# Kernel optimization log

Hardware: AMD Instinct MI355X
Metric: run time of the kernel (lower is better)

The kernel has to match this reference:

```python
import jax, jax.numpy as jnp
import numpy as np

B, H, N, D, M = 1, 4, 2048, 64, 256  # batch, heads, seq, dim_heads, nb_features
EPS = 1e-4


def _gaussian_orthogonal_random_matrix(nb_rows, nb_cols, seed=0):
    # scaling=1 path of the torch code: stacked transposed-Q orthogonal blocks,
    # scaled by sqrt(nb_cols).
    rng = np.random.default_rng(seed)
    blocks = []
    for _ in range(nb_rows // nb_cols):
        q, _ = np.linalg.qr(rng.standard_normal((nb_cols, nb_cols)))
        blocks.append(q.T)
    final = np.concatenate(blocks, axis=0)  # [nb_rows, nb_cols]
    return jnp.asarray(np.sqrt(float(nb_cols)) * final, dtype=jnp.float32)


def setup_inputs() -> dict:
    key = jax.random.key(0)
    kq, kk, kv = jax.random.split(key, 3)
    return {
        "q": jax.random.normal(kq, (B, H, N, D), dtype=jnp.float32),
        "k": jax.random.normal(kk, (B, H, N, D), dtype=jnp.float32),
        "v": jax.random.normal(kv, (B, H, N, D), dtype=jnp.float32),
        "projection_matrix": _gaussian_orthogonal_random_matrix(M, D),
    }


def _softmax_kernel(data, projection_matrix, is_query):
    # data: [B,H,N,D], projection_matrix: [M,D] -> features [B,H,N,M]
    data_normalizer = 1.0 / data.shape[-1] ** 0.25
    ratio = 1.0 / projection_matrix.shape[0] ** 0.5
    data_dash = jnp.einsum("bhnd,md->bhnm", data_normalizer * data, projection_matrix)
    diag_data = jnp.sum(data * data, axis=-1) * 0.5 * data_normalizer ** 2  # [B,H,N]
    diag_data = diag_data[..., None]  # [B,H,N,1]
    if is_query:
        stab = jnp.max(data_dash, axis=-1, keepdims=True)
    else:
        stab = jnp.max(data_dash)
    return ratio * (jnp.exp(data_dash - diag_data - stab) + EPS)


def _causal_linear_attention(q, k, v):
    # q,k: [B,H,N,M] features; v: [B,H,N,E]
    k_cumsum = jnp.cumsum(k, axis=-2)                       # [B,H,N,M]
    context = jnp.einsum("bhnm,bhne->bhnme", k, v)          # outer products
    context = jnp.cumsum(context, axis=-3)                  # cumulative over n
    context = context / k_cumsum[..., None]                 # [B,H,N,M,E]
    return jnp.einsum("bhnme,bhnm->bhne", context, q)


def reference(q, k, v, projection_matrix):
    q_feat = _softmax_kernel(q, projection_matrix, is_query=True)
    k_feat = _softmax_kernel(k, projection_matrix, is_query=False)
    return _causal_linear_attention(q_feat, k_feat, v)
```

## Files before the change

### kernel.cpp

```cpp
#include <hip/hip_runtime.h>
#include <math.h>

#define NH   4
#define SEQ  2048
#define DH   64
#define NF   256
#define ROWS (NH*SEQ)
#define DN    0.35355339059327373f
#define DIAGC 0.0625f
#define RATIO 0.0625f
#define EPSF  1e-4f

typedef __attribute__((ext_vector_type(8))) short bf8;
typedef __attribute__((ext_vector_type(4))) short bf4;
typedef __attribute__((ext_vector_type(4))) float f4;

static __device__ __forceinline__ unsigned short f2bf(float x) {
  union { float f; unsigned u; } v; v.f = x;
  unsigned r = v.u + 0x7FFF + ((v.u >> 16) & 1);
  return (unsigned short)(r >> 16);
}
static __device__ __forceinline__ float bf2f(unsigned short b) {
  union { unsigned u; float f; } v; v.u = ((unsigned)b) << 16;
  return v.f;
}

__global__ __launch_bounds__(256) void k_proj(const float* __restrict__ q,
    const float* __restrict__ k, const float* __restrict__ v,
    const float* __restrict__ P,
    unsigned short* __restrict__ qfb, float* __restrict__ dshd,
    float* __restrict__ bmax, unsigned short* __restrict__ vtb) {
  __shared__ float lds[64*65];
  const int b = blockIdx.x;
  if (b >= 1024) {
    const int cb = b - 1024;
    const int h = cb >> 5, n0 = (cb & 31) * 64;
    const int tid = threadIdx.x;
    for (int i = tid; i < 4096; i += 256) {
      int n = i >> 6, e = i & 63;
      lds[n*65 + e] = v[((size_t)h*SEQ + n0 + n)*DH + e];
    }
    __syncthreads();
    for (int i = tid; i < 4096; i += 256) {
      int e = i >> 6, n = i & 63;
      vtb[((size_t)h*DH + e)*SEQ + n0 + n] = f2bf(lds[n*65 + e]);
    }
    return;
  }
  const bool isq = b < 512;
  const int tile = isq ? b : b - 512;
  const int w = threadIdx.x >> 6, lane = threadIdx.x & 63;
  const int lr = lane & 15, g = lane >> 4;
  const float* x = (isq ? q : k) + (size_t)tile*16*DH;

  f4 a  = *(const f4*)(x + lr*DH + g*8);
  f4 bb = *(const f4*)(x + lr*DH + g*8 + 4);
  f4 c  = *(const f4*)(x + lr*DH + 32 + g*8);
  f4 d  = *(const f4*)(x + lr*DH + 32 + g*8 + 4);
  float ss = 0.f;
#pragma unroll
  for (int i = 0; i < 4; ++i) ss += a[i]*a[i] + bb[i]*bb[i] + c[i]*c[i] + d[i]*d[i];
  ss += __shfl_xor(ss, 16);
  ss += __shfl_xor(ss, 32);

  bf8 xh0, xh1, xl0, xl1;
#pragma unroll
  for (int i = 0; i < 4; ++i) {
    float v0 = DN*a[i], v1 = DN*bb[i], v2 = DN*c[i], v3 = DN*d[i];
    unsigned short h0 = f2bf(v0), h1 = f2bf(v1), h2 = f2bf(v2), h3 = f2bf(v3);
    xh0[i] = (short)h0; xh0[i+4] = (short)h1;
    xh1[i] = (short)h2; xh1[i+4] = (short)h3;
    xl0[i]   = (short)f2bf(v0 - bf2f(h0)); xl0[i+4] = (short)f2bf(v1 - bf2f(h1));
    xl1[i]   = (short)f2bf(v2 - bf2f(h2)); xl1[i+4] = (short)f2bf(v3 - bf2f(h3));
  }

  const int ct0 = w*4;
  f4 dsh[4];
#pragma unroll
  for (int cc = 0; cc < 4; ++cc) {
    const int ct = ct0 + cc;
    const float* prow = P + (ct*16 + lr)*DH + g*8;
    f4 p0 = *(const f4*)(prow);
    f4 p1 = *(const f4*)(prow + 4);
    f4 p2 = *(const f4*)(prow + 32);
    f4 p3 = *(const f4*)(prow + 36);
    bf8 bh0, bl0, bh1, bl1;
#pragma unroll
    for (int i = 0; i < 4; ++i) {
      unsigned short h0 = f2bf(p0[i]), h1 = f2bf(p1[i]);
      unsigned short h2 = f2bf(p2[i]), h3 = f2bf(p3[i]);
      bh0[i] = (short)h0; bh0[i+4] = (short)h1;
      bh1[i] = (short)h2; bh1[i+4] = (short)h3;
      bl0[i]   = (short)f2bf(p0[i] - bf2f(h0)); bl0[i+4] = (short)f2bf(p1[i] - bf2f(h1));
      bl1[i]   = (short)f2bf(p2[i] - bf2f(h2)); bl1[i+4] = (short)f2bf(p3[i] - bf2f(h3));
    }
    f4 acc = {0.f, 0.f, 0.f, 0.f};
    acc = __builtin_amdgcn_mfma_f32_16x16x32_bf16(xh0, bh0, acc, 0, 0, 0);
    acc = __builtin_amdgcn_mfma_f32_16x16x32_bf16(xh1, bh1, acc, 0, 0, 0);
    acc = __builtin_amdgcn_mfma_f32_16x16x32_bf16(xh0, bl0, acc, 0, 0, 0);
    acc = __builtin_amdgcn_mfma_f32_16x16x32_bf16(xh1, bl1, acc, 0, 0, 0);
    acc = __builtin_amdgcn_mfma_f32_16x16x32_bf16(xl0, bh0, acc, 0, 0, 0);
    acc = __builtin_amdgcn_mfma_f32_16x16x32_bf16(xl1, bh1, acc, 0, 0, 0);
    dsh[cc] = acc;
  }

  f4 mr;
#pragma unroll
  for (int r = 0; r < 4; ++r)
    mr[r] = fmaxf(fmaxf(dsh[0][r], dsh[1][r]), fmaxf(dsh[2][r], dsh[3][r]));
#pragma unroll
  for (int mk = 1; mk <= 8; mk <<= 1) {
#pragma unroll
    for (int r = 0; r < 4; ++r) mr[r] = fmaxf(mr[r], __shfl_xor(mr[r], mk));
  }
  if (lr == 0) {
#pragma unroll
    for (int r = 0; r < 4; ++r) lds[w*16 + 4*g + r] = mr[r];
  }
  __syncthreads();
  float rm[4], sr[4];
#pragma unroll
  for (int r = 0; r < 4; ++r) {
    rm[r] = fmaxf(fmaxf(lds[0*16 + 4*g + r], lds[1*16 + 4*g + r]),
                  fmaxf(lds[2*16 + 4*g + r], lds[3*16 + 4*g + r]));
    sr[r] = __shfl(ss, 4*g + r);
  }

  if (isq) {
    unsigned short* ob = qfb + (size_t)tile*16*NF;
#pragma unroll
    for (int cc = 0; cc < 4; ++cc) {
#pragma unroll
      for (int r = 0; r < 4; ++r)
        ob[(4*g + r)*NF + (ct0 + cc)*16 + lr] =
            f2bf(RATIO*(expf(dsh[cc][r] - (sr[r]*DIAGC + rm[r])) + EPSF));
    }
  } else {
    float* db = dshd + (size_t)tile*16*NF;
#pragma unroll
    for (int cc = 0; cc < 4; ++cc) {
#pragma unroll
      for (int r = 0; r < 4; ++r)
        db[(4*g + r)*NF + (ct0 + cc)*16 + lr] = dsh[cc][r] - sr[r]*DIAGC;
    }
    float tmax = fmaxf(fmaxf(rm[0], rm[1]), fmaxf(rm[2], rm[3]));
    tmax = fmaxf(tmax, __shfl_xor(tmax, 16));
    tmax = fmaxf(tmax, __shfl_xor(tmax, 32));
    if (w == 0 && lane == 0) bmax[tile] = tmax;
  }
}

__global__ __launch_bounds__(256) void k_feat2(const float* __restrict__ dshd,
    const float* __restrict__ bmax, unsigned short* __restrict__ kfb,
    unsigned short* __restrict__ kft, float* __restrict__ csum) {
  const int u = blockIdx.x, m = threadIdx.x;
  const int h = u >> 7, t = u & 127;
  __shared__ float red[256];
  red[m] = fmaxf(bmax[m], bmax[m + 256]);
  __syncthreads();
  for (int s = 128; s > 0; s >>= 1) {
    if (m < s) red[m] = fmaxf(red[m], red[m+s]);
    __syncthreads();
  }
  const float gg = red[0];
  const float* db = dshd + (size_t)u*16*NF + m;
  unsigned short* ob = kfb + (size_t)u*16*NF + m;
  float run = 0.f;
  bf8 k0, k1;
#pragma unroll
  for (int r = 0; r < 16; ++r) {
    unsigned short bv = f2bf(RATIO*(expf(db[r*NF] - gg) + EPSF));
    ob[r*NF] = bv;
    if (r < 8) k0[r] = (short)bv; else k1[r-8] = (short)bv;
    run += bf2f(bv);
  }
  csum[(size_t)u*NF + m] = run;
  unsigned short* kt = kft + ((size_t)(h*NF + m))*SEQ + t*16;
  *(bf8*)kt = k0;
  *(bf8*)(kt + 8) = k1;
}

__global__ __launch_bounds__(128) void k_state(
    const unsigned short* __restrict__ vtb, const unsigned short* __restrict__ kft,
    unsigned short* __restrict__ sthi, unsigned short* __restrict__ stlo,
    float* __restrict__ csum) {
  const int bx = blockIdx.x;
  if (bx >= 256) {
    if (threadIdx.x >= 64) return;
    const int h = bx - 256;
    const int m0 = threadIdx.x * 4;
    f4 run = {0.f, 0.f, 0.f, 0.f};
#pragma unroll 4
    for (int c = 0; c < 128; ++c) {
      float* p = csum + ((size_t)(h*128 + c))*NF + m0;
      f4 x = *(const f4*)p;
      *(f4*)p = run;
      run += x;
    }
    return;
  }
  __shared__ f4 bridge[64];
  const int wid = threadIdx.x >> 6, lane = threadIdx.x & 63;
  const int lr = lane & 15, g = lane >> 4;
  const int h = bx >> 6, et = (bx >> 4) & 3, mt = bx & 15;

  const unsigned short* vb = vtb + ((size_t)(h*DH + et*16 + lr))*SEQ;
  const unsigned short* kb = kft + ((size_t)(h*NF + mt*16 + lr))*SEQ;

  f4 cum = {0.f, 0.f, 0.f, 0.f};
  f4 loc[8];
  const int c0 = wid*8;
#pragma unroll
  for (int cc = 0; cc < 8; ++cc) {
    const int c = c0 + cc;
    if (wid == 0) {
      const size_t base = ((size_t)((h*16 + c)*64 + et*16 + 4*g))*NF + mt*16 + lr;
#pragma unroll
      for (int r = 0; r < 4; ++r) {
        unsigned short hi = f2bf(cum[r]);
        sthi[base + (size_t)r*NF] = hi;
        stlo[base + (size_t)r*NF] = f2bf(cum[r] - bf2f(hi));
      }
    } else {
      loc[cc] = cum;
    }
#pragma unroll
    for (int ks = 0; ks < 4; ++ks) {
      const int j0 = c*128 + ks*32 + g*8;
      bf8 xv = *(const bf8*)(vb + j0);
      bf8 ym = *(const bf8*)(kb + j0);
      cum = __builtin_amdgcn_mfma_f32_16x16x32_bf16(xv, ym, cum, 0, 0, 0);
    }
  }
  if (wid == 0) bridge[lane] = cum;
  __syncthreads();
  if (wid == 1) {
    f4 s8 = bridge[lane];
#pragma unroll
    for (int cc = 0; cc < 8; ++cc) {
      const int c = 8 + cc;
      f4 val = s8 + loc[cc];
      const size_t base = ((size_t)((h*16 + c)*64 + et*16 + 4*g))*NF + mt*16 + lr;
#pragma unroll
      for (int r = 0; r < 4; ++r) {
        unsigned short hi = f2bf(val[r]);
        sthi[base + (size_t)r*NF] = hi;
        stlo[base + (size_t)r*NF] = f2bf(val[r] - bf2f(hi));
      }
    }
  }
}

__global__ __launch_bounds__(64) void k_attn4(const unsigned short* __restrict__ qpb,
                                              const unsigned short* __restrict__ kfb,
                                              const unsigned short* __restrict__ vtb,
                                              const unsigned short* __restrict__ sthi,
                                              const unsigned short* __restrict__ stlo,
                                              const float* __restrict__ csum,
                                              float* __restrict__ out) {
  const int h = blockIdx.y;
  const int t = blockIdx.x;
  const int c = t >> 3;
  const int jc0 = c*8;
  const int nstage = (t & 7) + 1;
  const int lane = threadIdx.x;
  const int lr = lane & 15, g = lane >> 4;

  __shared__ __align__(16) char smem[18432];
  char* Ks = smem + 8192;
  char* Vs = smem + 16384;

  {
    const int u = h*128 + t;
    f4 run = *(const f4*)(csum + (size_t)u*NF + lane*4);
    const unsigned short* kfp = kfb + ((size_t)(h*SEQ + t*16))*NF + lane*4;
    const unsigned short* qfp = qpb + ((size_t)(h*SEQ + t*16))*NF + lane*4;
#pragma unroll
    for (int r = 0; r < 16; ++r) {
      bf4 kv = *(const bf4*)(kfp + (size_t)r*NF);
      bf4 qv = *(const bf4*)(qfp + (size_t)r*NF);
      unsigned short qp[4];
#pragma unroll
      for (int i = 0; i < 4; ++i) {
        run[i] += bf2f((unsigned short)kv[i]);
        qp[i] = f2bf(bf2f((unsigned short)qv[i]) / run[i]);
      }
      const int byte = (r*512 + lane*8) ^ ((r & 7) << 4);
      *(bf4*)(smem + byte) = *(bf4*)qp;
    }
  }

  bf8 qf[8];
#pragma unroll
  for (int kb = 0; kb < 8; ++kb) {
    const int byte = (lr*512 + g*16 + kb*64) ^ ((lr & 7) << 4);
    qf[kb] = *(const bf8*)(smem + byte);
  }

  const char* kTile = (const char*)(kfb + (size_t)h*SEQ*NF);
  const char* vTile = (const char*)(vtb + (size_t)h*DH*SEQ);

  int kw[8];
#pragma unroll
  for (int i = 0; i < 8; ++i) {
    const int ko = i*1024 + lane*16;
    kw[i] = ko ^ (((ko >> 9) & 7) << 4);
  }

  f4 sk[8], sv0, sv1;
  {
    const char* kt = kTile + (size_t)jc0*8192;
#pragma unroll
    for (int i = 0; i < 8; ++i) sk[i] = *(const f4*)(kt + i*1024 + lane*16);
    const char* vt = vTile + (size_t)lane*4096 + (size_t)jc0*32;
    sv0 = *(const f4*)(vt);
    sv1 = *(const f4*)(vt + 16);
  }

  f4 o0 = {0,0,0,0}, o1 = {0,0,0,0}, o2 = {0,0,0,0}, o3 = {0,0,0,0};
  {
    const unsigned short* SH = sthi + ((size_t)((h*16 + c)*64 + lr))*NF + g*8;
    const unsigned short* SL = stlo + ((size_t)((h*16 + c)*64 + lr))*NF + g*8;
#pragma unroll
    for (int ks = 0; ks < 8; ++ks) {
#pragma unroll
      for (int et = 0; et < 4; ++et) {
        bf8 bh = *(const bf8*)(SH + et*16*NF + ks*32);
        bf8 bl = *(const bf8*)(SL + et*16*NF + ks*32);
        f4 acc = (et == 0) ? o0 : (et == 1) ? o1 : (et == 2) ? o2 : o3;
        acc = __builtin_amdgcn_mfma_f32_16x16x32_bf16(qf[ks], bh, acc, 0, 0, 0);
        acc = __builtin_amdgcn_mfma_f32_16x16x32_bf16(qf[ks], bl, acc, 0, 0, 0);
        if (et == 0) o0 = acc; else if (et == 1) o1 = acc; else if (et == 2) o2 = acc; else o3 = acc;
      }
    }
  }

  for (int jj = 0; jj < nstage; ++jj) {
    const int j = jc0 + jj;
#pragma unroll
    for (int i = 0; i < 8; ++i) *(f4*)(Ks + kw[i]) = sk[i];
    *(f4*)(Vs + lane*32) = sv0;
    *(f4*)(Vs + lane*32 + 16) = sv1;
    if (jj + 1 < nstage) {
      const char* kt = kTile + (size_t)(j+1)*8192;
#pragma unroll
      for (int i = 0; i < 8; ++i) sk[i] = *(const f4*)(kt + i*1024 + lane*16);
      const char* vt = vTile + (size_t)lane*4096 + (size_t)(j+1)*32;
      sv0 = *(const f4*)(vt);
      sv1 = *(const f4*)(vt + 16);
    }
    bf8 kcs[8];
#pragma unroll
    for (int kb = 0; kb < 8; ++kb) {
      int off = (lr*512 + kb*64 + g*16) ^ ((lr & 7) << 4);
      kcs[kb] = *(const bf8*)(Ks + off);
    }
    f4 st = {0,0,0,0};
#pragma unroll
    for (int kb = 0; kb < 8; ++kb)
      st = __builtin_amdgcn_mfma_f32_16x16x32_bf16(kcs[kb], qf[kb], st, 0, 0, 0);
    if (j == t) {
#pragma unroll
      for (int rr = 0; rr < 4; ++rr) if (g*4 + rr > lr) st[rr] = 0.f;
    }
    bf8 sb = { (short)f2bf(st[0]), (short)f2bf(st[1]), (short)f2bf(st[2]), (short)f2bf(st[3]),
               (short)0, (short)0, (short)0, (short)0 };
#pragma unroll
    for (int eb = 0; eb < 4; ++eb) {
      bf4 v4 = *(const bf4*)(Vs + (eb*16 + lr)*32 + g*8);
      bf8 vf = { v4[0], v4[1], v4[2], v4[3], (short)0, (short)0, (short)0, (short)0 };
      f4 acc = (eb == 0) ? o0 : (eb == 1) ? o1 : (eb == 2) ? o2 : o3;
      acc = __builtin_amdgcn_mfma_f32_16x16x32_bf16(sb, vf, acc, 0, 0, 0);
      if (eb == 0) o0 = acc; else if (eb == 1) o1 = acc; else if (eb == 2) o2 = acc; else o3 = acc;
    }
  }

  float* ob = out + ((size_t)(h*SEQ + t*16))*DH;
#pragma unroll
  for (int rr = 0; rr < 4; ++rr) {
    ob[(size_t)(4*g + rr)*DH +  0 + lr] = o0[rr];
    ob[(size_t)(4*g + rr)*DH + 16 + lr] = o1[rr];
    ob[(size_t)(4*g + rr)*DH + 32 + lr] = o2[rr];
    ob[(size_t)(4*g + rr)*DH + 48 + lr] = o3[rr];
  }
}

extern "C" void kernel_launch(void* const* d_in, const int* in_sizes, int n_in,
                              void* d_out, int out_size, void* d_ws, size_t ws_size,
                              hipStream_t stream) {
  const float* q = (const float*)d_in[0];
  const float* k = (const float*)d_in[1];
  const float* v = (const float*)d_in[2];
  const float* P = (const float*)d_in[3];
  float* out = (float*)d_out;

  char* ws = (char*)d_ws;
  unsigned short* qfb  = (unsigned short*)(ws);
  unsigned short* kfb  = (unsigned short*)(ws + (4u<<20));
  unsigned short* vtb  = (unsigned short*)(ws + (8u<<20));
  unsigned short* kft  = (unsigned short*)(ws + (12u<<20));
  float* dshd   = (float*)(ws + (16u<<20));
  float* bmax   = (float*)(ws + (24u<<20));
  float* csum   = (float*)(ws + (25u<<20));
  unsigned short* sthi = (unsigned short*)(ws + (33u<<20));
  unsigned short* stlo = (unsigned short*)(ws + (36u<<20));

  k_proj  <<<1152, 256, 0, stream>>>(q, k, v, P, qfb, dshd, bmax, vtb);
  k_feat2 <<<512, 256, 0, stream>>>(dshd, bmax, kfb, kft, csum);
  k_state <<<260, 128, 0, stream>>>(vtb, kft, sthi, stlo, csum);
  k_attn4 <<<dim3(128, NH), 64, 0, stream>>>(qfb, kfb, vtb, sthi, stlo, csum, out);
}
```

Baseline: 54.34 us.

## Split attention block into two waves: inter-chunk state and intra-chunk causal

```diff
diff --git a/kernel.cpp b/kernel.cpp
--- a/kernel.cpp
+++ b/kernel.cpp
@@ -251,44 +251,47 @@
   }
 }
 
-__global__ __launch_bounds__(64) void k_attn4(const unsigned short* __restrict__ qpb,
-                                              const unsigned short* __restrict__ kfb,
-                                              const unsigned short* __restrict__ vtb,
-                                              const unsigned short* __restrict__ sthi,
-                                              const unsigned short* __restrict__ stlo,
-                                              const float* __restrict__ csum,
-                                              float* __restrict__ out) {
+__global__ __launch_bounds__(128) void k_attn5(const unsigned short* __restrict__ qpb,
+                                               const unsigned short* __restrict__ kfb,
+                                               const unsigned short* __restrict__ vtb,
+                                               const unsigned short* __restrict__ sthi,
+                                               const unsigned short* __restrict__ stlo,
+                                               const float* __restrict__ csum,
+                                               float* __restrict__ out) {
   const int h = blockIdx.y;
   const int t = blockIdx.x;
   const int c = t >> 3;
   const int jc0 = c*8;
   const int nstage = (t & 7) + 1;
-  const int lane = threadIdx.x;
+  const int tid = threadIdx.x;
+  const int wid = tid >> 6, lane = tid & 63;
   const int lr = lane & 15, g = lane >> 4;
 
-  __shared__ __align__(16) char smem[18432];
+  __shared__ __align__(16) char smem[22528];
   char* Ks = smem + 8192;
   char* Vs = smem + 16384;
+  float* MG = (float*)(smem + 18432);
 
   {
     const int u = h*128 + t;
-    f4 run = *(const f4*)(csum + (size_t)u*NF + lane*4);
-    const unsigned short* kfp = kfb + ((size_t)(h*SEQ + t*16))*NF + lane*4;
-    const unsigned short* qfp = qpb + ((size_t)(h*SEQ + t*16))*NF + lane*4;
+    const int m = tid*2;
+    float run0 = csum[(size_t)u*NF + m];
+    float run1 = csum[(size_t)u*NF + m + 1];
+    const unsigned short* kfp = kfb + ((size_t)(h*SEQ + t*16))*NF + m;
+    const unsigned short* qfp = qpb + ((size_t)(h*SEQ + t*16))*NF + m;
 #pragma unroll
     for (int r = 0; r < 16; ++r) {
-      bf4 kv = *(const bf4*)(kfp + (size_t)r*NF);
-      bf4 qv = *(const bf4*)(qfp + (size_t)r*NF);
-      unsigned short qp[4];
-#pragma unroll
-      for (int i = 0; i < 4; ++i) {
-        run[i] += bf2f((unsigned short)kv[i]);
-        qp[i] = f2bf(bf2f((unsigned short)qv[i]) / run[i]);
-      }
-      const int byte = (r*512 + lane*8) ^ ((r & 7) << 4);
-      *(bf4*)(smem + byte) = *(bf4*)qp;
-    }
-  }
+      unsigned kv = *(const unsigned*)(kfp + (size_t)r*NF);
+      unsigned qv = *(const unsigned*)(qfp + (size_t)r*NF);
+      run0 += bf2f((unsigned short)(kv & 0xffff));
+      run1 += bf2f((unsigned short)(kv >> 16));
+      unsigned short q0 = f2bf(bf2f((unsigned short)(qv & 0xffff)) / run0);
+      unsigned short q1 = f2bf(bf2f((unsigned short)(qv >> 16)) / run1);
+      const int byte = (r*512 + m*2) ^ ((r & 7) << 4);
+      *(unsigned*)(smem + byte) = (unsigned)q0 | ((unsigned)q1 << 16);
+    }
+  }
+  __syncthreads();
 
   bf8 qf[8];
 #pragma unroll
@@ -297,28 +300,70 @@
     qf[kb] = *(const bf8*)(smem + byte);
   }
 
-  const char* kTile = (const char*)(kfb + (size_t)h*SEQ*NF);
-  const char* vTile = (const char*)(vtb + (size_t)h*DH*SEQ);
-
-  int kw[8];
-#pragma unroll
-  for (int i = 0; i < 8; ++i) {
-    const int ko = i*1024 + lane*16;
-    kw[i] = ko ^ (((ko >> 9) & 7) << 4);
-  }
-
-  f4 sk[8], sv0, sv1;
-  {
-    const char* kt = kTile + (size_t)jc0*8192;
-#pragma unroll
-    for (int i = 0; i < 8; ++i) sk[i] = *(const f4*)(kt + i*1024 + lane*16);
-    const char* vt = vTile + (size_t)lane*4096 + (size_t)jc0*32;
-    sv0 = *(const f4*)(vt);
-    sv1 = *(const f4*)(vt + 16);
-  }
-
   f4 o0 = {0,0,0,0}, o1 = {0,0,0,0}, o2 = {0,0,0,0}, o3 = {0,0,0,0};
-  {
+
+  if (wid == 1) {
+    const char* kTile = (const char*)(kfb + (size_t)h*SEQ*NF);
+    const char* vTile = (const char*)(vtb + (size_t)h*DH*SEQ);
+    int kw[8];
+#pragma unroll
+    for (int i = 0; i < 8; ++i) {
+      const int ko = i*1024 + lane*16;
+      kw[i] = ko ^ (((ko >> 9) & 7) << 4);
+    }
+    f4 sk[8], sv0, sv1;
+    {
+      const char* kt = kTile + (size_t)jc0*8192;
+#pragma unroll
+      for (int i = 0; i < 8; ++i) sk[i] = *(const f4*)(kt + i*1024 + lane*16);
+      const char* vt = vTile + (size_t)lane*4096 + (size_t)jc0*32;
+      sv0 = *(const f4*)(vt);
+      sv1 = *(const f4*)(vt + 16);
+    }
+    for (int jj = 0; jj < nstage; ++jj) {
+      const int j = jc0 + jj;
+#pragma unroll
+      for (int i = 0; i < 8; ++i) *(f4*)(Ks + kw[i]) = sk[i];
+      *(f4*)(Vs + lane*32) = sv0;
+      *(f4*)(Vs + lane*32 + 16) = sv1;
+      if (jj + 1 < nstage) {
+        const char* kt = kTile + (size_t)(j+1)*8192;
+#pragma unroll
+        for (int i = 0; i < 8; ++i) sk[i] = *(const f4*)(kt + i*1024 + lane*16);
+        const char* vt = vTile + (size_t)lane*4096 + (size_t)(j+1)*32;
+        sv0 = *(const f4*)(vt);
+        sv1 = *(const f4*)(vt + 16);
+      }
+      bf8 kcs[8];
+#pragma unroll
+      for (int kb = 0; kb < 8; ++kb) {
+        int off = (lr*512 + kb*64 + g*16) ^ ((lr & 7) << 4);
+        kcs[kb] = *(const bf8*)(Ks + off);
+      }
+      f4 st = {0,0,0,0};
+#pragma unroll
+      for (int kb = 0; kb < 8; ++kb)
+        st = __builtin_amdgcn_mfma_f32_16x16x32_bf16(kcs[kb], qf[kb], st, 0, 0, 0);
+      if (j == t) {
+#pragma unroll
+        for (int rr = 0; rr < 4; ++rr) if (g*4 + rr > lr) st[rr] = 0.f;
+      }
+      bf8 sb = { (short)f2bf(st[0]), (short)f2bf(st[1]), (short)f2bf(st[2]), (short)f2bf(st[3]),
+                 (short)0, (short)0, (short)0, (short)0 };
+#pragma unroll
+      for (int eb = 0; eb < 4; ++eb) {
+        bf4 v4 = *(const bf4*)(Vs + (eb*16 + lr)*32 + g*8);
+        bf8 vf = { v4[0], v4[1], v4[2], v4[3], (short)0, (short)0, (short)0, (short)0 };
+        f4 acc = (eb == 0) ? o0 : (eb == 1) ? o1 : (eb == 2) ? o2 : o3;
+        acc = __builtin_amdgcn_mfma_f32_16x16x32_bf16(sb, vf, acc, 0, 0, 0);
+        if (eb == 0) o0 = acc; else if (eb == 1) o1 = acc; else if (eb == 2) o2 = acc; else o3 = acc;
+      }
+    }
+    *(f4*)(MG + (0*64 + lane)*4) = o0;
+    *(f4*)(MG + (1*64 + lane)*4) = o1;
+    *(f4*)(MG + (2*64 + lane)*4) = o2;
+    *(f4*)(MG + (3*64 + lane)*4) = o3;
+  } else {
     const unsigned short* SH = sthi + ((size_t)((h*16 + c)*64 + lr))*NF + g*8;
     const unsigned short* SL = stlo + ((size_t)((h*16 + c)*64 + lr))*NF + g*8;
 #pragma unroll
@@ -334,54 +379,21 @@
       }
     }
   }
-
-  for (int jj = 0; jj < nstage; ++jj) {
-    const int j = jc0 + jj;
-#pragma unroll
-    for (int i = 0; i < 8; ++i) *(f4*)(Ks + kw[i]) = sk[i];
-    *(f4*)(Vs + lane*32) = sv0;
-    *(f4*)(Vs + lane*32 + 16) = sv1;
-    if (jj + 1 < nstage) {
-      const char* kt = kTile + (size_t)(j+1)*8192;
-#pragma unroll
-      for (int i = 0; i < 8; ++i) sk[i] = *(const f4*)(kt + i*1024 + lane*16);
-      const char* vt = vTile + (size_t)lane*4096 + (size_t)(j+1)*32;
-      sv0 = *(const f4*)(vt);
-      sv1 = *(const f4*)(vt + 16);
-    }
-    bf8 kcs[8];
-#pragma unroll
-    for (int kb = 0; kb < 8; ++kb) {
-      int off = (lr*512 + kb*64 + g*16) ^ ((lr & 7) << 4);
-      kcs[kb] = *(const bf8*)(Ks + off);
-    }
-    f4 st = {0,0,0,0};
-#pragma unroll
-    for (int kb = 0; kb < 8; ++kb)
-      st = __builtin_amdgcn_mfma_f32_16x16x32_bf16(kcs[kb], qf[kb], st, 0, 0, 0);
-    if (j == t) {
-#pragma unroll
-      for (int rr = 0; rr < 4; ++rr) if (g*4 + rr > lr) st[rr] = 0.f;
-    }
-    bf8 sb = { (short)f2bf(st[0]), (short)f2bf(st[1]), (short)f2bf(st[2]), (short)f2bf(st[3]),
-               (short)0, (short)0, (short)0, (short)0 };
-#pragma unroll
-    for (int eb = 0; eb < 4; ++eb) {
-      bf4 v4 = *(const bf4*)(Vs + (eb*16 + lr)*32 + g*8);
-      bf8 vf = { v4[0], v4[1], v4[2], v4[3], (short)0, (short)0, (short)0, (short)0 };
-      f4 acc = (eb == 0) ? o0 : (eb == 1) ? o1 : (eb == 2) ? o2 : o3;
-      acc = __builtin_amdgcn_mfma_f32_16x16x32_bf16(sb, vf, acc, 0, 0, 0);
-      if (eb == 0) o0 = acc; else if (eb == 1) o1 = acc; else if (eb == 2) o2 = acc; else o3 = acc;
-    }
-  }
-
-  float* ob = out + ((size_t)(h*SEQ + t*16))*DH;
-#pragma unroll
-  for (int rr = 0; rr < 4; ++rr) {
-    ob[(size_t)(4*g + rr)*DH +  0 + lr] = o0[rr];
-    ob[(size_t)(4*g + rr)*DH + 16 + lr] = o1[rr];
-    ob[(size_t)(4*g + rr)*DH + 32 + lr] = o2[rr];
-    ob[(size_t)(4*g + rr)*DH + 48 + lr] = o3[rr];
+  __syncthreads();
+
+  if (wid == 0) {
+    o0 += *(const f4*)(MG + (0*64 + lane)*4);
+    o1 += *(const f4*)(MG + (1*64 + lane)*4);
+    o2 += *(const f4*)(MG + (2*64 + lane)*4);
+    o3 += *(const f4*)(MG + (3*64 + lane)*4);
+    float* ob = out + ((size_t)(h*SEQ + t*16))*DH;
+#pragma unroll
+    for (int rr = 0; rr < 4; ++rr) {
+      ob[(size_t)(4*g + rr)*DH +  0 + lr] = o0[rr];
+      ob[(size_t)(4*g + rr)*DH + 16 + lr] = o1[rr];
+      ob[(size_t)(4*g + rr)*DH + 32 + lr] = o2[rr];
+      ob[(size_t)(4*g + rr)*DH + 48 + lr] = o3[rr];
+    }
   }
 }
 
@@ -408,5 +420,5 @@
   k_proj  <<<1152, 256, 0, stream>>>(q, k, v, P, qfb, dshd, bmax, vtb);
   k_feat2 <<<512, 256, 0, stream>>>(dshd, bmax, kfb, kft, csum);
   k_state <<<260, 128, 0, stream>>>(vtb, kft, sthi, stlo, csum);
-  k_attn4 <<<dim3(128, NH), 64, 0, stream>>>(qfb, kfb, vtb, sthi, stlo, csum, out);
-}
+  k_attn5 <<<dim3(128, NH), 128, 0, stream>>>(qfb, kfb, vtb, sthi, stlo, csum, out);
+}
```

Result: faster. 52.22 us (-3.9%).
